# Kernel optimization log

Hardware: AMD Instinct MI355X
Metric: run time of the kernel (lower is better)

The kernel has to match this reference:

```python
import jax, jax.numpy as jnp
import numpy as np

# Module hyperparameters (init_kwargs)
NH = 254          # nHidden
NSTEP = 32        # MPC horizon
DT = 1.0 / 60.0   # del_t
EPS = 1e-4
PQ = 5.0
QV = 200.0
QA = 1.0
N_STATE = NH + 2  # hidden embedding + [position, velocity]
NBATCH = 256


def setup_inputs() -> dict:
    key = jax.random.key(0)
    k1, k2, k3, k4, k5, k6 = jax.random.split(key, 6)
    x = jax.random.normal(k1, (NBATCH, NH), dtype=jnp.float32)
    gripper_p = jax.random.normal(k2, (NBATCH,), dtype=jnp.float32)
    own_gripper_v = jax.random.normal(k3, (NBATCH,), dtype=jnp.float32)
    other_gripper_v = jax.random.normal(k4, (NBATCH,), dtype=jnp.float32)
    # Learned parameters (as in __init__): Af ~ U[0,1), Lq = tril(U[0,1))
    Af = jax.random.uniform(k5, (NH, 1), dtype=jnp.float32)
    Lq = jnp.tril(jax.random.uniform(k6, (NH, NH), dtype=jnp.float32))
    return {"x": x, "gripper_p": gripper_p, "own_gripper_v": own_gripper_v,
            "other_gripper_v": other_gripper_v, "Af": Af, "Lq": Lq}


def _mpc_forward(x, gripper_p, own_gripper_v, Af, Lq):
    n = N_STATE
    dt = x.dtype
    eye_n = jnp.eye(n, dtype=dt)

    # ---- Q0: [[Lq Lq^T + eps I, 0], [0, diag(0, Qv)]]  (n x n) ----
    Q0_tl = Lq @ Lq.T + EPS * jnp.eye(NH, dtype=dt)
    Q0 = jnp.zeros((n, n), dt).at[:NH, :NH].set(Q0_tl).at[NH + 1, NH + 1].set(QV)
    w = jnp.ones((NSTEP,), dt).at[-1].set(PQ)        # final-step weight Pq
    Q0_stack = w[:, None, None] * Q0                 # [NSTEP, n, n]
    Q_dia = jax.scipy.linalg.block_diag(*Q0_stack)   # [NSTEP*n, NSTEP*n]

    # ---- A0: [[I, 0, Af], [0, 1, dt], [0, 0, 1]] ----
    A0 = jnp.zeros((n, n), dt)
    A0 = A0.at[:NH, :NH].set(jnp.eye(NH, dtype=dt)).at[:NH, NH + 1].set(Af[:, 0])
    A0 = A0.at[NH, NH].set(1.0).at[NH, NH + 1].set(DT).at[NH + 1, NH + 1].set(1.0)

    # ---- powers A0^1..A0^NSTEP via scan (replaces the Python power loop) ----
    def step(carry, _):
        nxt = carry @ A0
        return nxt, nxt
    _, Pk = jax.lax.scan(step, eye_n, None, length=NSTEP)   # Pk[k] = A0^{k+1}
    P = jnp.concatenate([eye_n[None], Pk], axis=0)          # A0^0 .. A0^NSTEP
    T_ = Pk.reshape(NSTEP * n, n)                           # vstack(A0^1..A0^NSTEP)

    # ---- AN_: block lower-triangular Toeplitz, block (i,j) = A0^{i-j} for j<=i ----
    d = jnp.arange(NSTEP)[:, None] - jnp.arange(NSTEP)[None, :]
    blocks = jnp.where((d >= 0)[:, :, None, None],
                       P[jnp.clip(d, 0, NSTEP)], jnp.zeros((), dt))  # [NSTEP,NSTEP,n,n]
    AN_ = blocks.transpose(0, 2, 1, 3).reshape(NSTEP * n, NSTEP * n)

    B0 = jnp.zeros((n, 1), dt).at[NH, 0].set(0.5 * DT * DT).at[NH + 1, 0].set(DT)
    B_dia = jax.scipy.linalg.block_diag(*jnp.broadcast_to(B0, (NSTEP, n, 1)))

    S_ = AN_ @ B_dia                                        # [NSTEP*n, NSTEP]
    QS = Q_dia @ S_                                         # [NSTEP*n, NSTEP]
    Q_final = 2.0 * (QA * jnp.eye(NSTEP, dtype=dt) + S_.T @ QS) \
              + EPS * jnp.eye(NSTEP, dtype=dt)
    p_final = 2.0 * (T_.T @ QS)                             # [n, NSTEP]

    # ---- batch state x0 = [x, gripper_p, own_gripper_v] ----
    x0 = jnp.concatenate([x, gripper_p[:, None], own_gripper_v[:, None]], axis=1)
    p_x0 = x0 @ p_final                                     # [B, NSTEP]

    # QPFunction with G=0, h=0, no equalities -> unconstrained QP:
    # u = argmin 0.5 u^T Q_final u + p_x0^T u = -Q_final^{-1} p_x0
    u = -jnp.linalg.solve(Q_final, p_x0.T).T                # [B, NSTEP]

    # x_predict = S u + T x0 ; output picks position component (index NH) per step
    x_pred = u @ S_.T + x0 @ T_.T                           # [B, NSTEP*n]
    posi = x_pred.reshape(-1, NSTEP, n)[:, :, NH]           # [B, NSTEP]
    return posi


def reference(x, gripper_p, own_gripper_v, other_gripper_v, Af, Lq):
    # other_gripper_v is accepted but unused in the active forward path (as in source)
    return _mpc_forward(x, gripper_p, own_gripper_v, Af, Lq)
```

## Files before the change

### kernel.cpp

```cpp
#include <hip/hip_runtime.h>

#define NH 254
#define NSTEP 32
#define NB 256

constexpr float  FEPS = 1e-4f;
constexpr double DDT  = 1.0 / 60.0;
constexpr double DQV  = 200.0;
constexpr double DPQ  = 5.0;
constexpr double DQA  = 1.0;
constexpr double DEPS = 1e-4;

__global__ __launch_bounds__(256) void k_phase1(const float* __restrict__ Lq,
                                                const float* __restrict__ Af,
                                                float* __restrict__ partial) {
    const int k  = threadIdx.x;
    const int b  = blockIdx.x;
    const int i0 = b * 8;
    const int iend = (i0 + 8 < NH) ? i0 + 8 : NH;
    float acc = 0.f;
    if (k < NH) {
        int ibeg = (k > i0) ? k : i0;
        for (int i = ibeg; i < iend; ++i)
            acc += Lq[i * NH + k] * Af[i];
    }
    partial[b * 256 + k] = acc;
}

__global__ __launch_bounds__(256) void k_phase2(const float* __restrict__ Lq,
                                                const float* __restrict__ Af,
                                                const float* __restrict__ partial,
                                                float* __restrict__ g,
                                                float* __restrict__ coef) {
    __shared__ float t_sh[256];
    const int k = threadIdx.x;
    const int lane = k & 63;
    const int w = k >> 6;

    float tk = 0.f;
    #pragma unroll
    for (int b = 0; b < 32; ++b) tk += partial[b * 256 + k];
    t_sh[k] = tk;
    __syncthreads();

    if (blockIdx.x < 32) {
        const int i0 = blockIdx.x * 8;
        for (int rr = 0; rr < 2; ++rr) {
            const int i = i0 + 2 * w + rr;
            if (i >= NH) break;
            float acc = 0.f;
            #pragma unroll
            for (int c4 = 0; c4 < 4; ++c4) {
                int kk = lane + 64 * c4;
                if (kk <= i) acc += Lq[i * NH + kk] * t_sh[kk];
            }
            #pragma unroll
            for (int off = 32; off; off >>= 1) acc += __shfl_xor(acc, off, 64);
            if (lane == 0) g[i] = acc + FEPS * Af[i];
        }
        return;
    }

    __shared__ double red[4];
    __shared__ double M[32][34];
    __shared__ double ua[32], ub[32];

    double v = 0.0;
    if (k < NH) {
        double td = (double)t_sh[k];
        double ad = (double)Af[k];
        v = td * td + DEPS * ad * ad;
    }
    #pragma unroll
    for (int off = 32; off; off >>= 1) v += __shfl_xor(v, off, 64);
    if (lane == 0) red[w] = v;
    __syncthreads();
    const double c = red[0] + red[1] + red[2] + red[3];

    for (int e = k; e < 1024; e += 256) {
        const int j1 = e >> 5, j2 = e & 31;
        const int m = (j1 > j2) ? j1 : j2;
        double s = 0.0;
        for (int kk = m; kk < 32; ++kk) {
            const double wk = (kk == 31) ? DPQ : 1.0;
            s += wk * ((double)(kk - j1) * (double)(kk - j2) * c + DQV);
        }
        M[j1][j2] = 2.0 * DDT * DDT * s + ((j1 == j2) ? (2.0 * DQA + DEPS) : 0.0);
    }
    if (k < 32) {
        const int j = k;
        double sa = 0.0, sb = 0.0;
        for (int kk = j; kk < 32; ++kk) {
            const double wk = (kk == 31) ? DPQ : 1.0;
            sa += wk * (double)(kk - j);
            sb += wk * ((double)(kk + 1) * (double)(kk - j) * c + DQV);
        }
        M[j][32] = 2.0 * DDT * sa;
        M[j][33] = 2.0 * DDT * sb;
    }
    __syncthreads();

    const int r  = k & 31;
    const int cg = k >> 5;
    for (int p = 0; p < 32; ++p) {
        const double f = M[r][p] / M[p][p];
        if (r != p) {
            for (int cc = cg; cc < 34; cc += 8)
                if (cc > p) M[r][cc] -= f * M[p][cc];
        }
        __syncthreads();
    }

    if (k < 32) {
        ua[k] = -M[k][32] / M[k][k];
        ub[k] = -M[k][33] / M[k][k];
    }
    __syncthreads();

    if (k < 32) {
        const int i = k;
        double ca = 0.0, cb = 0.0;
        for (int j = 0; j <= i; ++j) {
            const double wgt = (double)(i - j) + 0.5;
            ca += wgt * ua[j];
            cb += wgt * ub[j];
        }
        ca *= DDT * DDT;
        cb *= DDT * DDT;
        coef[i]      = (float)ca;
        coef[32 + i] = (float)((double)(i + 1) * DDT + cb);
    }
}

__global__ __launch_bounds__(64) void k_phase3(const float* __restrict__ x,
                                               const float* __restrict__ gp,
                                               const float* __restrict__ gv,
                                               const float* __restrict__ g,
                                               const float* __restrict__ coef,
                                               float* __restrict__ out) {
    const int b = blockIdx.x;
    const int lane = threadIdx.x;
    float acc = 0.f;
    #pragma unroll
    for (int c4 = 0; c4 < 4; ++c4) {
        const int kk = lane + 64 * c4;
        if (kk < NH) acc += x[b * NH + kk] * g[kk];
    }
    #pragma unroll
    for (int off = 32; off; off >>= 1) acc += __shfl_xor(acc, off, 64);
    if (lane < 32) {
        out[b * NSTEP + lane] = gp[b] + gv[b] * coef[32 + lane] + acc * coef[lane];
    }
}

extern "C" void kernel_launch(void* const* d_in, const int* in_sizes, int n_in,
                              void* d_out, int out_size, void* d_ws, size_t ws_size,
                              hipStream_t stream) {
    const float* x  = (const float*)d_in[0];
    const float* gp = (const float*)d_in[1];
    const float* gv = (const float*)d_in[2];
    const float* Af = (const float*)d_in[4];
    const float* Lq = (const float*)d_in[5];
    float* out = (float*)d_out;

    float* ws      = (float*)d_ws;
    float* partial = ws;
    float* g       = ws + 32 * 256;
    float* coef    = g + 256;

    k_phase1<<<32, 256, 0, stream>>>(Lq, Af, partial);
    k_phase2<<<33, 256, 0, stream>>>(Lq, Af, partial, g, coef);
    k_phase3<<<NB, 64, 0, stream>>>(x, gp, gv, g, coef, out);
}
```

Measured before the change: 91.56 us.

## Fuse the Lq^T·Af reduction into the coefficient kernel and drop one launch

The separate partial-sum kernel and its workspace round trip are removed. Each of the 33 blocks now computes t = Lq^T·Af on its own, looping serially over rows with Af staged in shared memory. This removes one kernel launch and the global partial buffer. In exchange the Lq triangle is read redundantly by every block, and each thread runs a longer serial loop.

New measurement: 99.59 us. 8.8% more time.

```diff
diff --git a/kernel.cpp b/kernel.cpp
--- a/kernel.cpp
+++ b/kernel.cpp
@@ -11,36 +11,26 @@
 constexpr double DQA  = 1.0;
 constexpr double DEPS = 1e-4;
 
-__global__ __launch_bounds__(256) void k_phase1(const float* __restrict__ Lq,
-                                                const float* __restrict__ Af,
-                                                float* __restrict__ partial) {
-    const int k  = threadIdx.x;
-    const int b  = blockIdx.x;
-    const int i0 = b * 8;
-    const int iend = (i0 + 8 < NH) ? i0 + 8 : NH;
+__global__ __launch_bounds__(256) void k_tg(const float* __restrict__ Lq,
+                                            const float* __restrict__ Af,
+                                            float* __restrict__ g,
+                                            float* __restrict__ coef) {
+    __shared__ float t_sh[256];
+    __shared__ float af_sh[256];
+    const int k    = threadIdx.x;
+    const int lane = k & 63;
+    const int w    = k >> 6;
+
+    af_sh[k] = (k < NH) ? Af[k] : 0.f;
+    __syncthreads();
+
     float acc = 0.f;
     if (k < NH) {
-        int ibeg = (k > i0) ? k : i0;
-        for (int i = ibeg; i < iend; ++i)
-            acc += Lq[i * NH + k] * Af[i];
+        #pragma unroll 8
+        for (int i = 64 * w; i < NH; ++i)
+            acc += Lq[i * NH + k] * af_sh[i];
     }
-    partial[b * 256 + k] = acc;
-}
-
-__global__ __launch_bounds__(256) void k_phase2(const float* __restrict__ Lq,
-                                                const float* __restrict__ Af,
-                                                const float* __restrict__ partial,
-                                                float* __restrict__ g,
-                                                float* __restrict__ coef) {
-    __shared__ float t_sh[256];
-    const int k = threadIdx.x;
-    const int lane = k & 63;
-    const int w = k >> 6;
-
-    float tk = 0.f;
-    #pragma unroll
-    for (int b = 0; b < 32; ++b) tk += partial[b * 256 + k];
-    t_sh[k] = tk;
+    t_sh[k] = acc;
     __syncthreads();
 
     if (blockIdx.x < 32) {
@@ -48,15 +38,15 @@
         for (int rr = 0; rr < 2; ++rr) {
             const int i = i0 + 2 * w + rr;
             if (i >= NH) break;
-            float acc = 0.f;
+            float a2 = 0.f;
             #pragma unroll
             for (int c4 = 0; c4 < 4; ++c4) {
                 int kk = lane + 64 * c4;
-                if (kk <= i) acc += Lq[i * NH + kk] * t_sh[kk];
+                if (kk <= i) a2 += Lq[i * NH + kk] * t_sh[kk];
             }
             #pragma unroll
-            for (int off = 32; off; off >>= 1) acc += __shfl_xor(acc, off, 64);
-            if (lane == 0) g[i] = acc + FEPS * Af[i];
+            for (int off = 32; off; off >>= 1) a2 += __shfl_xor(a2, off, 64);
+            if (lane == 0) g[i] = a2 + FEPS * Af[i];
         }
         return;
     }
@@ -68,7 +58,7 @@
     double v = 0.0;
     if (k < NH) {
         double td = (double)t_sh[k];
-        double ad = (double)Af[k];
+        double ad = (double)af_sh[k];
         v = td * td + DEPS * ad * ad;
     }
     #pragma unroll
@@ -132,12 +122,12 @@
     }
 }
 
-__global__ __launch_bounds__(64) void k_phase3(const float* __restrict__ x,
-                                               const float* __restrict__ gp,
-                                               const float* __restrict__ gv,
-                                               const float* __restrict__ g,
-                                               const float* __restrict__ coef,
-                                               float* __restrict__ out) {
+__global__ __launch_bounds__(64) void k_out(const float* __restrict__ x,
+                                            const float* __restrict__ gp,
+                                            const float* __restrict__ gv,
+                                            const float* __restrict__ g,
+                                            const float* __restrict__ coef,
+                                            float* __restrict__ out) {
     const int b = blockIdx.x;
     const int lane = threadIdx.x;
     float acc = 0.f;
@@ -163,12 +153,10 @@
     const float* Lq = (const float*)d_in[5];
     float* out = (float*)d_out;
 
-    float* ws      = (float*)d_ws;
-    float* partial = ws;
-    float* g       = ws + 32 * 256;
-    float* coef    = g + 256;
+    float* ws   = (float*)d_ws;
+    float* g    = ws;
+    float* coef = ws + 256;
 
-    k_phase1<<<32, 256, 0, stream>>>(Lq, Af, partial);
-    k_phase2<<<33, 256, 0, stream>>>(Lq, Af, partial, g, coef);
-    k_phase3<<<NB, 64, 0, stream>>>(x, gp, gv, g, coef, out);
+    k_tg<<<33, 256, 0, stream>>>(Lq, Af, g, coef);
+    k_out<<<NB, 64, 0, stream>>>(x, gp, gv, g, coef, out);
 }
```
